# Kernel optimization log

Measured on AMD Instinct MI355X. Metric: run time of the kernel, lower is better.

## Reference

```python
import jax, jax.numpy as jnp
import numpy as np

NEG = -1e9  # effective -inf in log space (finite to keep grads NaN-free)


def _forward_lattice(theta, A):
    """alpha[b,i,j,s]: log-prob of all alignments reaching cell (i,j) in state s.
    States: 0=match (diag move), 1=insert-x (down move), 2=insert-y (right move).
    alpha[i,j,s] = theta[i,j,s] + LSE_k(alpha[i-ds,j-dj,k] + A[k,s]).
    Start: only the match contribution at (0,0) gets log-prob 0."""
    B, N, M, S = theta.shape
    j_is0 = (jnp.arange(M) == 0)  # [M]

    def row_step(prev_row, xs):
        theta_row, i = xs  # theta_row: [B, M, S]
        # diag predecessor alpha[i-1, j-1, :]
        diag = jnp.concatenate(
            [jnp.full((B, 1, S), NEG, theta_row.dtype), prev_row[:, :-1]], axis=1)
        lse_m = jax.nn.logsumexp(diag + A[:, None, :, 0], axis=-1)      # [B, M]
        lse_m = jnp.where((i == 0) & j_is0[None, :], 0.0, lse_m)        # start at (0,0)
        lse_x = jax.nn.logsumexp(prev_row + A[:, None, :, 1], axis=-1)  # [B, M]
        m_vals = theta_row[:, :, 0] + lse_m
        x_vals = theta_row[:, :, 1] + lse_x
        th_y = theta_row[:, :, 2]

        def col_step(left, cxs):
            # left: alpha[i, j-1, :] -> [B, S]
            m_j, x_j, ty_j = cxs  # each [B]
            y_j = ty_j + jax.nn.logsumexp(left + A[:, :, 2], axis=-1)
            cell = jnp.stack([m_j, x_j, y_j], axis=-1)  # [B, S]
            return cell, cell

        left0 = jnp.full((B, S), NEG, theta_row.dtype)
        _, row = jax.lax.scan(col_step, left0, (m_vals.T, x_vals.T, th_y.T))
        row = jnp.transpose(row, (1, 0, 2))  # [B, M, S]
        return row, row

    prev0 = jnp.full((B, M, S), NEG, theta.dtype)
    _, alpha = jax.lax.scan(row_step, prev0, (jnp.swapaxes(theta, 0, 1), jnp.arange(N)))
    return jnp.swapaxes(alpha, 0, 1)  # [B, N, M, S]


def _backward_lattice(theta, A):
    """beta[b,i,j,s]: log-prob of all alignment suffixes from (i,j) in state s.
    beta[i,j,s] = LSE( A[s,0]+theta[i+1,j+1,0]+beta[i+1,j+1,0],
                       A[s,1]+theta[i+1,j,1]  +beta[i+1,j,1],
                       A[s,2]+theta[i,j+1,2]  +beta[i,j+1,2] ),  beta[N-1,M-1,:] = 0.
    Computed as a forward scan on the flipped grid with u = beta + theta."""
    B, N, M, S = theta.shape
    theta_f = theta[:, ::-1, ::-1]
    j_is0 = (jnp.arange(M) == 0)

    def row_step(u_prev, xs):
        th_row, p = xs  # th_row: [B, M, S] (flipped coords)
        t_m = jnp.concatenate(
            [jnp.full((B, 1), NEG, th_row.dtype), u_prev[:, :-1, 0]], axis=1)  # [B, M]
        t_x = u_prev[:, :, 1]  # [B, M]

        def col_step(left_u2, cxs):
            tm_j, tx_j, th_j, j0 = cxs  # [B], [B], [B,S], scalar bool
            v = jnp.stack([tm_j, tx_j, left_u2], axis=-1)     # [B, S] over successor k
            g = jax.nn.logsumexp(A + v[:, None, :], axis=-1)  # [B, S]
            g = jnp.where((p == 0) & j0, 0.0, g)              # terminal cell
            u = g + th_j
            return u[:, 2], (g, u)

        left0 = jnp.full((B,), NEG, th_row.dtype)
        _, (g_row, u_row) = jax.lax.scan(
            col_step, left0, (t_m.T, t_x.T, jnp.swapaxes(th_row, 0, 1), j_is0))
        return jnp.transpose(u_row, (1, 0, 2)), jnp.transpose(g_row, (1, 0, 2))

    u0 = jnp.full((B, M, S), NEG, theta.dtype)
    _, g = jax.lax.scan(row_step, u0, (jnp.swapaxes(theta_f, 0, 1), jnp.arange(N)))
    g = jnp.swapaxes(g, 0, 1)  # [B, N, M, S] flipped coords
    return g[:, ::-1, ::-1]


def setup_inputs() -> dict:
    key = jax.random.key(0)
    k1, k2 = jax.random.split(key)
    B, N, M, S = 256, 128, 128, 3
    theta = jax.random.normal(k1, (B, N, M, S), dtype=jnp.float32)
    A = jax.random.normal(k2, (B, S, S), dtype=jnp.float32)
    return {"theta": theta, "A": A}


def reference(theta, A):
    # Baum-Welch: posterior log-marginals gamma = alpha + beta - logZ
    alpha = _forward_lattice(theta, A)
    beta = _backward_lattice(theta, A)
    logZ = jax.nn.logsumexp(alpha[:, -1, -1, :], axis=-1)  # [B]
    return alpha + beta - logZ[:, None, None, None]
```

## Files before the change

### kernel.cpp

```cpp
#include <hip/hip_runtime.h>

#define HNEG (-1000000000.0f)
#define HNEG2 (-1.44269504e9f)
#define INVLN2 1.44269504088896341f
#define LN2F 0.69314718055994531f

constexpr int Nc = 128;
constexpr int Mc = 128;
constexpr int CELLS = Nc * Mc * 3;

__device__ __forceinline__ float ex2(float x) {
  return __builtin_amdgcn_exp2f(x);
}
__device__ __forceinline__ float lg2(float x) {
  return __builtin_amdgcn_logf(x);
}

__device__ __host__ constexpr int dpoff(int d) {
  return d <= 128 ? (d * (d + 1)) / 2 + ((d + 1) >> 1)
                  : 16448 - ((255 - d) * (256 - d)) / 2 + ((d - 127) >> 1);
}
__device__ __forceinline__ int dlod(int d) { return d > 127 ? d - 127 : 0; }
__device__ __forceinline__ int sidx(int d, int j) {
  const int lo = dlod(d);
  return dpoff(d) + j - lo + (lo & 1);
}
__device__ __forceinline__ int sidx_u(int d) {
  const int lo = dlod(d);
  return dpoff(d) - lo + (lo & 1);
}
constexpr int PCELLS = 16512;
constexpr int PFLOATS = PCELLS * 3;
constexpr int AWSTRIDE = CELLS + 16;

__device__ __forceinline__ float lse3(float a, float b, float c) {
  float mx = fmaxf(fmaxf(a, b), c);
  return mx + __logf(__expf(a - mx) + __expf(b - mx) + __expf(c - mx));
}

__device__ __forceinline__ float shr1f(float src, float fill) {
  return __int_as_float(__builtin_amdgcn_update_dpp(
      __float_as_int(fill), __float_as_int(src), 0x138, 0xF, 0xF, false));
}

__device__ __forceinline__ void st3_even(float* o, float a, float b, float c) {
  *(float2*)o = make_float2(a, b);
  o[2] = c;
}
__device__ __forceinline__ void st3_odd(float* o, float a, float b, float c) {
  o[0] = a;
  *(float2*)(o + 1) = make_float2(b, c);
}

__global__ __launch_bounds__(256) void transpose_kernel(
    const float* __restrict__ theta, float* __restrict__ thd) {
  const int b = blockIdx.x;
  const int tile = blockIdx.y;
  const int i0 = (tile >> 1) * 64, j0 = (tile & 1) * 64;
  const int t = threadIdx.x;
  __shared__ float lds[64 * 192];
  float4* lds4 = (float4*)lds;
  const float4* src4 = (const float4*)(theta + (size_t)b * CELLS);
  float* dst = thd + (size_t)b * PFLOATS;
  const int cbase = (j0 >> 6) * 48;
  for (int f = t; f < 64 * 48; f += 256) {
    const int r = f / 48, c4 = f - r * 48;
    lds4[f] = src4[(size_t)(i0 + r) * 96 + cbase + c4];
  }
  __syncthreads();
  const int g = t >> 6, w = t & 63;
  for (int ld = g; ld < 127; ld += 4) {
    const int d = i0 + j0 + ld;
    const int ljlo = ld > 63 ? ld - 63 : 0;
    const int ljhi = ld < 63 ? ld : 63;
    const int L = (ljhi - ljlo + 1) * 3;
    const int base = sidx(d, j0 + ljlo) * 3;
    for (int e = w; e < L; e += 64) {
      const int lj = ljlo + e / 3, s = e - (e / 3) * 3;
      dst[base + e] = lds[(ld - lj) * 192 + lj * 3 + s] * INVLN2;
    }
  }
}

#define DECL6(p) float p##0, p##1, p##2, p##3, p##4, p##5


#define F2LOAD(P, dd) do {                                                     \
    const int dc_ = (dd) > 254 ? 254 : (dd);                                   \
    const int su_ = __builtin_amdgcn_readfirstlane(sidx_u(dc_));               \
    const float2* p2_ = (const float2*)thd + ((su_ * 3) >> 1) + 3 * l;         \
    const float2 la_ = p2_[0], lb_ = p2_[1], lc_ = p2_[2];                     \
    P##0 = la_.x; P##1 = la_.y; P##2 = lb_.x;                                  \
    P##3 = lb_.y; P##4 = lc_.x; P##5 = lc_.y;                                  \
  } while (0)

#define F2STEP(P, dd) do {                                                     \
    const int iA_ = (dd) - jA, iB_ = (dd) - jB;                                \
    const bool okA_ = (unsigned)iA_ < (unsigned)Nc;                            \
    const bool okB_ = (unsigned)iB_ < (unsigned)Nc;                            \
    const float g0 = mS2 + lg2(wS20 * E00 + wS21 * E10 + wS22 * E20);          \
    const float g1 = mPA + lg2(wPA0 * E01 + wPA1 * E11 + wPA2 * E21);          \
    const float g2 = mS1 + lg2(wS10 * E02 + wS11 * E12 + wS12 * E22);          \
    const float cA0 = okA_ ? P##0 + g0 : HNEG2;                                \
    const float cA1 = okA_ ? P##1 + g1 : HNEG2;                                \
    const float cA2 = okA_ ? P##2 + g2 : HNEG2;                                \
    st3_even(okA_ ? aw + (iA_ * Mc + jA) * 3 : dmpE, cA0, cA1, cA2);           \
    const float h0 = mPP + lg2(wPP0 * E00 + wPP1 * E10 + wPP2 * E20);          \
    const float h1 = mPB + lg2(wPB0 * E01 + wPB1 * E11 + wPB2 * E21);          \
    const float h2 = mPA + lg2(wPA0 * E02 + wPA1 * E12 + wPA2 * E22);          \
    const float cB0 = okB_ ? P##3 + h0 : HNEG2;                                \
    const float cB1 = okB_ ? P##4 + h1 : HNEG2;                                \
    const float cB2 = okB_ ? P##5 + h2 : HNEG2;                                \
    st3_odd(okB_ ? aw + (iB_ * Mc + jB) * 3 : dmpO, cB0, cB1, cB2);            \
    const float mA_ = fmaxf(fmaxf(cA0, cA1), cA2);                             \
    const float a0_ = ex2(cA0 - mA_), a1_ = ex2(cA1 - mA_),                    \
                a2_ = ex2(cA2 - mA_);                                          \
    const float mB_ = fmaxf(fmaxf(cB0, cB1), cB2);                             \
    const float b0_ = ex2(cB0 - mB_), b1_ = ex2(cB1 - mB_),                    \
                b2_ = ex2(cB2 - mB_);                                          \
    mPP = mPA; wPP0 = wPA0; wPP1 = wPA1; wPP2 = wPA2;                          \
    mPA = mA_; wPA0 = a0_; wPA1 = a1_; wPA2 = a2_;                             \
    mPB = mB_; wPB0 = b0_; wPB1 = b1_; wPB2 = b2_;                             \
    mS2 = mS1; wS20 = wS10; wS21 = wS11; wS22 = wS12;                          \
    mS1 = shr1f(mB_, HNEG2);                                                   \
    wS10 = shr1f(b0_, 1.f); wS11 = shr1f(b1_, 1.f); wS12 = shr1f(b2_, 1.f);    \
  } while (0)

#define B2LOADL(Pt, dd) do {                                                   \
    int dor_ = 254 - (dd); if (dor_ < 0) dor_ = 0;                             \
    const int su_ = __builtin_amdgcn_readfirstlane(sidx_u(dor_));              \
    const float2* p2_ =                                                        \
        (const float2*)thd + ((su_ * 3) >> 1) + 3 * (63 - l);                  \
    const float2 la_ = p2_[0], lb_ = p2_[1], lc_ = p2_[2];                     \
    Pt##3 = la_.x; Pt##4 = la_.y; Pt##5 = lb_.x;                               \
    Pt##0 = lb_.y; Pt##1 = lc_.x; Pt##2 = lc_.y;                               \
  } while (0)

#define B2STEPL(Pt, dd) do {                                                   \
    const int iA_ = Nc - 1 - (dd) + jA;                                        \
    const int iB_ = Nc - 1 - (dd) + jB;                                        \
    const bool okA_ = (unsigned)iA_ < (unsigned)Nc;                            \
    const bool okB_ = (unsigned)iB_ < (unsigned)Nc;                            \
    float uA0, uA1, uA2, uB0, uB1, uB2;                                        \
    {                                                                          \
      const float v0 = S2u0, v1 = pAu1, v2 = S1u2;                             \
      const float mv = fmaxf(fmaxf(v0, v1), v2);                               \
      const float w0 = ex2(v0 - mv), w1 = ex2(v1 - mv), w2 = ex2(v2 - mv);     \
      float g0 = mv + lg2(w0 * E00 + w1 * E01 + w2 * E02);                     \
      float g1 = mv + lg2(w0 * E10 + w1 * E11 + w2 * E12);                     \
      float g2 = mv + lg2(w0 * E20 + w1 * E21 + w2 * E22);                     \
      if ((dd) == 0 && l == 0) { g0 = 0.f; g1 = 0.f; g2 = 0.f; }               \
      uA0 = okA_ ? g0 + Pt##0 : HNEG2;                                         \
      uA1 = okA_ ? g1 + Pt##1 : HNEG2;                                         \
      uA2 = okA_ ? g2 + Pt##2 : HNEG2;                                         \
      st3_odd(okA_ ? ob + (iA_ * Mc + jjA) * 3 : dmpO, g0, g1, g2);            \
    }                                                                          \
    {                                                                          \
      const float v0 = ppAu0, v1 = pBu1, v2 = pAu2;                            \
      const float mv = fmaxf(fmaxf(v0, v1), v2);                               \
      const float w0 = ex2(v0 - mv), w1 = ex2(v1 - mv), w2 = ex2(v2 - mv);     \
      const float g0 = mv + lg2(w0 * E00 + w1 * E01 + w2 * E02);               \
      const float g1 = mv + lg2(w0 * E10 + w1 * E11 + w2 * E12);               \
      const float g2 = mv + lg2(w0 * E20 + w1 * E21 + w2 * E22);               \
      uB0 = okB_ ? g0 + Pt##3 : HNEG2;                                         \
      uB1 = okB_ ? g1 + Pt##4 : HNEG2;                                         \
      uB2 = okB_ ? g2 + Pt##5 : HNEG2;                                         \
      st3_even(okB_ ? ob + (iB_ * Mc + jjB) * 3 : dmpE, g0, g1, g2);           \
    }                                                                          \
    ppAu0 = pAu0; pAu0 = uA0; pAu1 = uA1; pAu2 = uA2; pBu1 = uB1;              \
    S2u0 = S1u0;                                                               \
    S1u0 = shr1f(uB0, HNEG2);                                                  \
    S1u2 = shr1f(uB2, HNEG2);                                                  \
  } while (0)

__global__ __launch_bounds__(128, 1) void fb2_kernel(
    const float* __restrict__ thd_, const float* __restrict__ A,
    float* __restrict__ aw_, float* __restrict__ logZ_ws,
    float* __restrict__ ob_) {
  const int b = blockIdx.x;
  const int wave = threadIdx.x >> 6;
  const int l = threadIdx.x & 63;
  const float* thd = thd_ + (size_t)b * PFLOATS;
  const float* Ab = A + b * 9;
  const float E00 = __expf(Ab[0]), E01 = __expf(Ab[1]), E02 = __expf(Ab[2]);
  const float E10 = __expf(Ab[3]), E11 = __expf(Ab[4]), E12 = __expf(Ab[5]);
  const float E20 = __expf(Ab[6]), E21 = __expf(Ab[7]), E22 = __expf(Ab[8]);

  const int jA = 2 * l, jB = 2 * l + 1;
  float* dpad = aw_ + (size_t)b * AWSTRIDE + CELLS;

  if (wave == 0) {
    float* aw = aw_ + (size_t)b * AWSTRIDE;
    float* dmpE = dpad;
    float* dmpO = dpad + 3;

    float mPA = HNEG2, wPA0 = 1.f, wPA1 = 1.f, wPA2 = 1.f;
    float mPB = HNEG2, wPB0 = 1.f, wPB1 = 1.f, wPB2 = 1.f;
    float mPP = HNEG2, wPP0 = 1.f, wPP1 = 1.f, wPP2 = 1.f;
    float mS1 = HNEG2, wS10 = 1.f, wS11 = 1.f, wS12 = 1.f;
    float mS2 = HNEG2, wS20 = 1.f, wS21 = 1.f, wS22 = 1.f;
    if (l == 0) { mS2 = 0.f; wS20 = 1.0f / E00; wS21 = 0.f; wS22 = 0.f; }

    DECL6(xt0); DECL6(xt1); DECL6(xt2); DECL6(xt3);
    DECL6(yt0); DECL6(yt1); DECL6(yt2); DECL6(yt3);

    F2LOAD(xt0, 0); F2LOAD(xt1, 1); F2LOAD(xt2, 2); F2LOAD(xt3, 3);
    F2LOAD(yt0, 4); F2LOAD(yt1, 5); F2LOAD(yt2, 6); F2LOAD(yt3, 7);

    for (int t = 0; t < 31; ++t) {
      const int d0 = 8 * t;
      F2STEP(xt0, d0 + 0); F2STEP(xt1, d0 + 1); F2STEP(xt2, d0 + 2); F2STEP(xt3, d0 + 3);
      F2LOAD(xt0, d0 + 8); F2LOAD(xt1, d0 + 9); F2LOAD(xt2, d0 + 10); F2LOAD(xt3, d0 + 11);
      F2STEP(yt0, d0 + 4); F2STEP(yt1, d0 + 5); F2STEP(yt2, d0 + 6); F2STEP(yt3, d0 + 7);
      F2LOAD(yt0, d0 + 12); F2LOAD(yt1, d0 + 13); F2LOAD(yt2, d0 + 14); F2LOAD(yt3, d0 + 15);
    }
    F2STEP(xt0, 248); F2STEP(xt1, 249); F2STEP(xt2, 250); F2STEP(xt3, 251);
    F2STEP(yt0, 252); F2STEP(yt1, 253); F2STEP(yt2, 254);
    if (l == 63) logZ_ws[b] = mPB + lg2(wPB0 + wPB1 + wPB2);
  } else {
    float* ob = ob_ + (size_t)b * CELLS;
    const int jjA = Mc - 1 - jA, jjB = Mc - 1 - jB;
    float* dmpE = dpad + 8;
    float* dmpO = dpad + 11;

    float pAu0 = HNEG2, pAu1 = HNEG2, pAu2 = HNEG2;
    float ppAu0 = HNEG2, pBu1 = HNEG2;
    float S1u0 = HNEG2, S1u2 = HNEG2, S2u0 = HNEG2;

    DECL6(xt0); DECL6(xt1); DECL6(xt2); DECL6(xt3);
    DECL6(yt0); DECL6(yt1); DECL6(yt2); DECL6(yt3);

    B2LOADL(xt0, 0); B2LOADL(xt1, 1); B2LOADL(xt2, 2); B2LOADL(xt3, 3);
    B2LOADL(yt0, 4); B2LOADL(yt1, 5); B2LOADL(yt2, 6); B2LOADL(yt3, 7);

    for (int t = 0; t < 31; ++t) {
      const int d0 = 8 * t;
      B2STEPL(xt0, d0 + 0); B2STEPL(xt1, d0 + 1);
      B2STEPL(xt2, d0 + 2); B2STEPL(xt3, d0 + 3);
      B2LOADL(xt0, d0 + 8); B2LOADL(xt1, d0 + 9);
      B2LOADL(xt2, d0 + 10); B2LOADL(xt3, d0 + 11);
      B2STEPL(yt0, d0 + 4); B2STEPL(yt1, d0 + 5);
      B2STEPL(yt2, d0 + 6); B2STEPL(yt3, d0 + 7);
      B2LOADL(yt0, d0 + 12); B2LOADL(yt1, d0 + 13);
      B2LOADL(yt2, d0 + 14); B2LOADL(yt3, d0 + 15);
    }
    B2STEPL(xt0, 248); B2STEPL(xt1, 249); B2STEPL(xt2, 250); B2STEPL(xt3, 251);
    B2STEPL(yt0, 252); B2STEPL(yt1, 253); B2STEPL(yt2, 254);
  }
}

__global__ __launch_bounds__(256) void combine_kernel(
    const float4* __restrict__ aw4, const float* __restrict__ logZ_ws,
    float4* __restrict__ out4) {
  const int b = blockIdx.x;
  const float lz = logZ_ws[b];
  const int off = blockIdx.y * 1024 + threadIdx.x;
  const size_t ab = (size_t)b * (AWSTRIDE / 4);
  const size_t obx = (size_t)b * 12288;
#pragma unroll
  for (int k = 0; k < 4; ++k) {
    const size_t i = off + (size_t)k * 256;
    const float4 a = aw4[ab + i];
    const float4 g = out4[obx + i];
    out4[obx + i] =
        make_float4((a.x + g.x - lz) * LN2F, (a.y + g.y - lz) * LN2F,
                    (a.z + g.z - lz) * LN2F, (a.w + g.w - lz) * LN2F);
  }
}

__global__ __launch_bounds__(128) void fwd_fb(const float* __restrict__ theta,
                                              const float* __restrict__ A,
                                              float* __restrict__ out) {
  const int b = blockIdx.x;
  const int j = threadIdx.x;
  const float* th = theta + (size_t)b * CELLS;
  float* ob = out + (size_t)b * CELLS;

  __shared__ float sA[9];
  __shared__ float ring[3][Mc + 1][3];
  if (j < 9) sA[j] = A[b * 9 + j];
  {
    float* rf = &ring[0][0][0];
    for (int t = j; t < 3 * (Mc + 1) * 3; t += Mc) rf[t] = HNEG;
  }
  __syncthreads();
  const float A00 = sA[0], A01 = sA[1], A02 = sA[2];
  const float A10 = sA[3], A11 = sA[4], A12 = sA[5];
  const float A20 = sA[6], A21 = sA[7], A22 = sA[8];

  float p0 = HNEG, p1 = HNEG, p2 = HNEG;
  float tc0 = 0.f, tc1 = 0.f, tc2 = 0.f, tn0 = 0.f, tn1 = 0.f, tn2 = 0.f;
  if (j == 0) { tc0 = th[0]; tc1 = th[1]; tc2 = th[2]; }
  if (j <= 1) {
    const int i1 = 1 - j;
    const float* p = th + (i1 * Mc + j) * 3;
    tn0 = p[0]; tn1 = p[1]; tn2 = p[2];
  }
  int s0 = 0, s1 = 2, s2 = 1;
  for (int d = 0; d < Nc + Mc - 1; ++d) {
    const int i = d - j;
    float tf0 = 0.f, tf1 = 0.f, tf2 = 0.f;
    const int ip = i + 2;
    if (ip >= 0 && ip < Nc) {
      const float* p = th + (ip * Mc + j) * 3;
      tf0 = p[0]; tf1 = p[1]; tf2 = p[2];
    }
    float c0 = HNEG, c1 = HNEG, c2 = HNEG;
    if (i >= 0 && i < Nc) {
      const float* nd1 = ring[s1][j];
      const float* nd2 = ring[s2][j];
      float lm = lse3(nd2[0] + A00, nd2[1] + A10, nd2[2] + A20);
      if (i == 0 && j == 0) lm = 0.0f;
      float lx = lse3(p0 + A01, p1 + A11, p2 + A21);
      float ly = lse3(nd1[0] + A02, nd1[1] + A12, nd1[2] + A22);
      c0 = tc0 + lm; c1 = tc1 + lx; c2 = tc2 + ly;
      float* o = ob + (i * Mc + j) * 3;
      o[0] = c0; o[1] = c1; o[2] = c2;
    }
    float* w = ring[s0][j + 1];
    w[0] = c0; w[1] = c1; w[2] = c2;
    __syncthreads();
    p0 = c0; p1 = c1; p2 = c2;
    tc0 = tn0; tc1 = tn1; tc2 = tn2;
    tn0 = tf0; tn1 = tf1; tn2 = tf2;
    const int t = s2; s2 = s1; s1 = s0; s0 = t;
  }
}

__global__ __launch_bounds__(128) void bwd_fb(const float* __restrict__ theta,
                                              const float* __restrict__ A,
                                              float* __restrict__ ob_) {
  const int b = blockIdx.x;
  const int q = threadIdx.x;
  const float* th = theta + (size_t)b * CELLS;
  float* ob = ob_ + (size_t)b * CELLS;

  __shared__ float sA[9];
  __shared__ float ring[3][Mc + 1][3];
  __shared__ float sZ;
  if (q < 9) sA[q] = A[b * 9 + q];
  {
    float* rf = &ring[0][0][0];
    for (int t = q; t < 3 * (Mc + 1) * 3; t += Mc) rf[t] = HNEG;
  }
  if (q == 0) {
    sZ = lse3(ob[(Nc * Mc - 1) * 3 + 0], ob[(Nc * Mc - 1) * 3 + 1],
              ob[(Nc * Mc - 1) * 3 + 2]);
  }
  __syncthreads();
  const float A00 = sA[0], A01 = sA[1], A02 = sA[2];
  const float A10 = sA[3], A11 = sA[4], A12 = sA[5];
  const float A20 = sA[6], A21 = sA[7], A22 = sA[8];
  const float logZ = sZ;

  const int jj = Mc - 1 - q;
  float pu1 = HNEG;
  float tc0 = 0.f, tc1 = 0.f, tc2 = 0.f, tn0 = 0.f, tn1 = 0.f, tn2 = 0.f;
  float ac0 = 0.f, ac1 = 0.f, ac2 = 0.f, an0 = 0.f, an1 = 0.f, an2 = 0.f;
  if (q == 0) {
    const float* p = th + ((Nc - 1) * Mc + jj) * 3;
    tc0 = p[0]; tc1 = p[1]; tc2 = p[2];
    const float* a = ob + ((Nc - 1) * Mc + jj) * 3;
    ac0 = a[0]; ac1 = a[1]; ac2 = a[2];
  }
  if (q <= 1) {
    const int i1 = Nc - 2 + q;
    const float* p = th + (i1 * Mc + jj) * 3;
    tn0 = p[0]; tn1 = p[1]; tn2 = p[2];
    const float* a = ob + (i1 * Mc + jj) * 3;
    an0 = a[0]; an1 = a[1]; an2 = a[2];
  }
  int s0 = 0, s1 = 2, s2 = 1;
  for (int d = 0; d < Nc + Mc - 1; ++d) {
    const int p = d - q;
    const int i = Nc - 1 - p;
    float tf0 = 0.f, tf1 = 0.f, tf2 = 0.f, af0 = 0.f, af1 = 0.f, af2 = 0.f;
    const int ipf = i - 2;
    if (ipf >= 0 && ipf < Nc) {
      const float* pp = th + (ipf * Mc + jj) * 3;
      tf0 = pp[0]; tf1 = pp[1]; tf2 = pp[2];
      const float* aa = ob + (ipf * Mc + jj) * 3;
      af0 = aa[0]; af1 = aa[1]; af2 = aa[2];
    }
    float u0 = HNEG, u1 = HNEG, u2 = HNEG;
    if (p >= 0 && p < Nc) {
      const float* nd1 = ring[s1][q];
      const float* nd2 = ring[s2][q];
      const float v0 = nd2[0];
      const float v1 = pu1;
      const float v2 = nd1[2];
      float g0 = lse3(A00 + v0, A01 + v1, A02 + v2);
      float g1 = lse3(A10 + v0, A11 + v1, A12 + v2);
      float g2 = lse3(A20 + v0, A21 + v1, A22 + v2);
      if (p == 0 && q == 0) { g0 = 0.0f; g1 = 0.0f; g2 = 0.0f; }
      u0 = g0 + tc0; u1 = g1 + tc1; u2 = g2 + tc2;
      float* o = ob + (i * Mc + jj) * 3;
      o[0] = ac0 + g0 - logZ;
      o[1] = ac1 + g1 - logZ;
      o[2] = ac2 + g2 - logZ;
    }
    float* w = ring[s0][q + 1];
    w[0] = u0; w[1] = u1; w[2] = u2;
    __syncthreads();
    pu1 = u1;
    tc0 = tn0; tc1 = tn1; tc2 = tn2;
    tn0 = tf0; tn1 = tf1; tn2 = tf2;
    ac0 = an0; ac1 = an1; ac2 = an2;
    an0 = af0; an1 = af1; an2 = af2;
    const int t = s2; s2 = s1; s1 = s0; s0 = t;
  }
}

extern "C" void kernel_launch(void* const* d_in, const int* in_sizes, int n_in,
                              void* d_out, int out_size, void* d_ws, size_t ws_size,
                              hipStream_t stream) {
  const float* theta = (const float*)d_in[0];
  const float* A = (const float*)d_in[1];
  float* out = (float*)d_out;
  const int B = in_sizes[1] / 9;

  const size_t need = (size_t)B * (PFLOATS + AWSTRIDE + 1) * 4;
  if (ws_size >= need) {
    float* thd = (float*)d_ws;
    float* aw = thd + (size_t)B * PFLOATS;
    float* logZ_ws = aw + (size_t)B * AWSTRIDE;
    transpose_kernel<<<dim3(B, 4), dim3(256), 0, stream>>>(theta, thd);
    fb2_kernel<<<dim3(B), dim3(128), 0, stream>>>(thd, A, aw, logZ_ws, out);
    combine_kernel<<<dim3(B, 12), dim3(256), 0, stream>>>(
        (const float4*)aw, logZ_ws, (float4*)out);
  } else {
    fwd_fb<<<dim3(B), dim3(128), 0, stream>>>(theta, A, out);
    bwd_fb<<<dim3(B), dim3(128), 0, stream>>>(theta, A, out);
  }
}
```

Measured before the change: 204.0 us.

## Split forward and backward lattice across two waves each with LDS ring handoff

Moves the fused forward/backward kernel from one wave per direction, where each lane handled two columns, to two waves per direction, where each lane handles one column. The second wave runs one 8-diagonal block behind the first and receives boundary column state through a small shared-memory ring buffer. Block-wide barriers after every 8-diagonal block keep the two waves in step. This halves the serial work per lane and doubles the waves per workgroup, at the cost of 33 barriers, LDS traffic, and unaligned scalar stores in place of the paired vector stores.

Result: slower. 211.0 us (+3.4%).

```diff
diff --git a/kernel.cpp b/kernel.cpp
--- a/kernel.cpp
+++ b/kernel.cpp
@@ -41,15 +41,6 @@
 __device__ __forceinline__ float shr1f(float src, float fill) {
   return __int_as_float(__builtin_amdgcn_update_dpp(
       __float_as_int(fill), __float_as_int(src), 0x138, 0xF, 0xF, false));
-}
-
-__device__ __forceinline__ void st3_even(float* o, float a, float b, float c) {
-  *(float2*)o = make_float2(a, b);
-  o[2] = c;
-}
-__device__ __forceinline__ void st3_odd(float* o, float a, float b, float c) {
-  o[0] = a;
-  *(float2*)(o + 1) = make_float2(b, c);
 }
 
 __global__ __launch_bounds__(256) void transpose_kernel(
@@ -82,103 +73,121 @@
   }
 }
 
-#define DECL6(p) float p##0, p##1, p##2, p##3, p##4, p##5
-
-
-#define F2LOAD(P, dd) do {                                                     \
+#define DECL3(p) float p##0, p##1, p##2
+
+
+#define FLOAD(TH, dd) do {                                                     \
     const int dc_ = (dd) > 254 ? 254 : (dd);                                   \
     const int su_ = __builtin_amdgcn_readfirstlane(sidx_u(dc_));               \
-    const float2* p2_ = (const float2*)thd + ((su_ * 3) >> 1) + 3 * l;         \
-    const float2 la_ = p2_[0], lb_ = p2_[1], lc_ = p2_[2];                     \
-    P##0 = la_.x; P##1 = la_.y; P##2 = lb_.x;                                  \
-    P##3 = lb_.y; P##4 = lc_.x; P##5 = lc_.y;                                  \
-  } while (0)
-
-#define F2STEP(P, dd) do {                                                     \
-    const int iA_ = (dd) - jA, iB_ = (dd) - jB;                                \
-    const bool okA_ = (unsigned)iA_ < (unsigned)Nc;                            \
-    const bool okB_ = (unsigned)iB_ < (unsigned)Nc;                            \
-    const float g0 = mS2 + lg2(wS20 * E00 + wS21 * E10 + wS22 * E20);          \
-    const float g1 = mPA + lg2(wPA0 * E01 + wPA1 * E11 + wPA2 * E21);          \
-    const float g2 = mS1 + lg2(wS10 * E02 + wS11 * E12 + wS12 * E22);          \
-    const float cA0 = okA_ ? P##0 + g0 : HNEG2;                                \
-    const float cA1 = okA_ ? P##1 + g1 : HNEG2;                                \
-    const float cA2 = okA_ ? P##2 + g2 : HNEG2;                                \
-    st3_even(okA_ ? aw + (iA_ * Mc + jA) * 3 : dmpE, cA0, cA1, cA2);           \
-    const float h0 = mPP + lg2(wPP0 * E00 + wPP1 * E10 + wPP2 * E20);          \
-    const float h1 = mPB + lg2(wPB0 * E01 + wPB1 * E11 + wPB2 * E21);          \
-    const float h2 = mPA + lg2(wPA0 * E02 + wPA1 * E12 + wPA2 * E22);          \
-    const float cB0 = okB_ ? P##3 + h0 : HNEG2;                                \
-    const float cB1 = okB_ ? P##4 + h1 : HNEG2;                                \
-    const float cB2 = okB_ ? P##5 + h2 : HNEG2;                                \
-    st3_odd(okB_ ? aw + (iB_ * Mc + jB) * 3 : dmpO, cB0, cB1, cB2);            \
-    const float mA_ = fmaxf(fmaxf(cA0, cA1), cA2);                             \
-    const float a0_ = ex2(cA0 - mA_), a1_ = ex2(cA1 - mA_),                    \
-                a2_ = ex2(cA2 - mA_);                                          \
-    const float mB_ = fmaxf(fmaxf(cB0, cB1), cB2);                             \
-    const float b0_ = ex2(cB0 - mB_), b1_ = ex2(cB1 - mB_),                    \
-                b2_ = ex2(cB2 - mB_);                                          \
-    mPP = mPA; wPP0 = wPA0; wPP1 = wPA1; wPP2 = wPA2;                          \
-    mPA = mA_; wPA0 = a0_; wPA1 = a1_; wPA2 = a2_;                             \
-    mPB = mB_; wPB0 = b0_; wPB1 = b1_; wPB2 = b2_;                             \
-    mS2 = mS1; wS20 = wS10; wS21 = wS11; wS22 = wS12;                          \
-    mS1 = shr1f(mB_, HNEG2);                                                   \
-    wS10 = shr1f(b0_, 1.f); wS11 = shr1f(b1_, 1.f); wS12 = shr1f(b2_, 1.f);    \
-  } while (0)
-
-#define B2LOADL(Pt, dd) do {                                                   \
+    const float* p_ = thd + su_ * 3 + 3 * j;                                   \
+    TH##0 = p_[0]; TH##1 = p_[1]; TH##2 = p_[2];                               \
+  } while (0)
+
+#define FSTEP(TH, dd) do {                                                     \
+    float4 hv_;                                                                \
+    if (isB && l == 0) hv_ = *(const float4*)&ringF[(dd) & 31][0];             \
+    const int i_ = (dd) - j;                                                   \
+    const bool ok_ = (unsigned)i_ < (unsigned)Nc;                              \
+    const float g0 = S2m + lg2(S2w0 * E00 + S2w1 * E10 + S2w2 * E20);          \
+    const float g1 = Pm + lg2(Pw0 * E01 + Pw1 * E11 + Pw2 * E21);              \
+    const float g2 = S1m + lg2(S1w0 * E02 + S1w1 * E12 + S1w2 * E22);          \
+    const float c0 = ok_ ? TH##0 + g0 : HNEG2;                                 \
+    const float c1 = ok_ ? TH##1 + g1 : HNEG2;                                 \
+    const float c2 = ok_ ? TH##2 + g2 : HNEG2;                                 \
+    float* o_ = ok_ ? aw + (i_ * Mc + j) * 3 : dmp;                            \
+    o_[0] = c0; o_[1] = c1; o_[2] = c2;                                        \
+    const float m_ = fmaxf(fmaxf(c0, c1), c2);                                 \
+    const float w0_ = ex2(c0 - m_), w1_ = ex2(c1 - m_), w2_ = ex2(c2 - m_);    \
+    if (!isB && l == 63)                                                       \
+      *(float4*)&ringF[(dd) & 31][0] = make_float4(m_, w0_, w1_, w2_);         \
+    S2m = S1m; S2w0 = S1w0; S2w1 = S1w1; S2w2 = S1w2;                          \
+    float nm_ = shr1f(m_, HNEG2);                                              \
+    float n0_ = shr1f(w0_, 1.f), n1_ = shr1f(w1_, 1.f), n2_ = shr1f(w2_, 1.f); \
+    if (isB && l == 0) { nm_ = hv_.x; n0_ = hv_.y; n1_ = hv_.z; n2_ = hv_.w; } \
+    S1m = nm_; S1w0 = n0_; S1w1 = n1_; S1w2 = n2_;                             \
+    Pm = m_; Pw0 = w0_; Pw1 = w1_; Pw2 = w2_;                                  \
+  } while (0)
+
+#define BLOAD(TH, dd) do {                                                     \
     int dor_ = 254 - (dd); if (dor_ < 0) dor_ = 0;                             \
     const int su_ = __builtin_amdgcn_readfirstlane(sidx_u(dor_));              \
-    const float2* p2_ =                                                        \
-        (const float2*)thd + ((su_ * 3) >> 1) + 3 * (63 - l);                  \
-    const float2 la_ = p2_[0], lb_ = p2_[1], lc_ = p2_[2];                     \
-    Pt##3 = la_.x; Pt##4 = la_.y; Pt##5 = lb_.x;                               \
-    Pt##0 = lb_.y; Pt##1 = lc_.x; Pt##2 = lc_.y;                               \
-  } while (0)
-
-#define B2STEPL(Pt, dd) do {                                                   \
-    const int iA_ = Nc - 1 - (dd) + jA;                                        \
-    const int iB_ = Nc - 1 - (dd) + jB;                                        \
-    const bool okA_ = (unsigned)iA_ < (unsigned)Nc;                            \
-    const bool okB_ = (unsigned)iB_ < (unsigned)Nc;                            \
-    float uA0, uA1, uA2, uB0, uB1, uB2;                                        \
-    {                                                                          \
-      const float v0 = S2u0, v1 = pAu1, v2 = S1u2;                             \
-      const float mv = fmaxf(fmaxf(v0, v1), v2);                               \
-      const float w0 = ex2(v0 - mv), w1 = ex2(v1 - mv), w2 = ex2(v2 - mv);     \
-      float g0 = mv + lg2(w0 * E00 + w1 * E01 + w2 * E02);                     \
-      float g1 = mv + lg2(w0 * E10 + w1 * E11 + w2 * E12);                     \
-      float g2 = mv + lg2(w0 * E20 + w1 * E21 + w2 * E22);                     \
-      if ((dd) == 0 && l == 0) { g0 = 0.f; g1 = 0.f; g2 = 0.f; }               \
-      uA0 = okA_ ? g0 + Pt##0 : HNEG2;                                         \
-      uA1 = okA_ ? g1 + Pt##1 : HNEG2;                                         \
-      uA2 = okA_ ? g2 + Pt##2 : HNEG2;                                         \
-      st3_odd(okA_ ? ob + (iA_ * Mc + jjA) * 3 : dmpO, g0, g1, g2);            \
-    }                                                                          \
-    {                                                                          \
-      const float v0 = ppAu0, v1 = pBu1, v2 = pAu2;                            \
-      const float mv = fmaxf(fmaxf(v0, v1), v2);                               \
-      const float w0 = ex2(v0 - mv), w1 = ex2(v1 - mv), w2 = ex2(v2 - mv);     \
-      const float g0 = mv + lg2(w0 * E00 + w1 * E01 + w2 * E02);               \
-      const float g1 = mv + lg2(w0 * E10 + w1 * E11 + w2 * E12);               \
-      const float g2 = mv + lg2(w0 * E20 + w1 * E21 + w2 * E22);               \
-      uB0 = okB_ ? g0 + Pt##3 : HNEG2;                                         \
-      uB1 = okB_ ? g1 + Pt##4 : HNEG2;                                         \
-      uB2 = okB_ ? g2 + Pt##5 : HNEG2;                                         \
-      st3_even(okB_ ? ob + (iB_ * Mc + jjB) * 3 : dmpE, g0, g1, g2);           \
-    }                                                                          \
-    ppAu0 = pAu0; pAu0 = uA0; pAu1 = uA1; pAu2 = uA2; pBu1 = uB1;              \
+    const float* p_ = thd + su_ * 3 + 3 * jj;                                  \
+    TH##0 = p_[0]; TH##1 = p_[1]; TH##2 = p_[2];                               \
+  } while (0)
+
+#define BSTEP(TH, dd) do {                                                     \
+    float2 hv_;                                                                \
+    if (isB && l == 0) hv_ = *(const float2*)&ringB[(dd) & 31][0];             \
+    const int i_ = Nc - 1 - (dd) + q;                                          \
+    const bool ok_ = (unsigned)i_ < (unsigned)Nc;                              \
+    const float v0 = S2u0, v1 = pu1, v2 = S1u2;                                \
+    const float mv = fmaxf(fmaxf(v0, v1), v2);                                 \
+    const float w0_ = ex2(v0 - mv), w1_ = ex2(v1 - mv), w2_ = ex2(v2 - mv);    \
+    float g0 = mv + lg2(w0_ * E00 + w1_ * E01 + w2_ * E02);                    \
+    float g1 = mv + lg2(w0_ * E10 + w1_ * E11 + w2_ * E12);                    \
+    float g2 = mv + lg2(w0_ * E20 + w1_ * E21 + w2_ * E22);                    \
+    if ((dd) == 0 && !isB && l == 0) { g0 = 0.f; g1 = 0.f; g2 = 0.f; }         \
+    const float u0 = ok_ ? g0 + TH##0 : HNEG2;                                 \
+    const float u1 = ok_ ? g1 + TH##1 : HNEG2;                                 \
+    const float u2 = ok_ ? g2 + TH##2 : HNEG2;                                 \
+    float* o_ = ok_ ? ob + (i_ * Mc + jj) * 3 : dmp;                           \
+    o_[0] = g0; o_[1] = g1; o_[2] = g2;                                        \
+    if (!isB && l == 63)                                                       \
+      *(float2*)&ringB[(dd) & 31][0] = make_float2(u0, u2);                    \
+    pu1 = u1;                                                                  \
     S2u0 = S1u0;                                                               \
-    S1u0 = shr1f(uB0, HNEG2);                                                  \
-    S1u2 = shr1f(uB2, HNEG2);                                                  \
-  } while (0)
-
-__global__ __launch_bounds__(128, 1) void fb2_kernel(
+    float n0_ = shr1f(u0, HNEG2), n2_ = shr1f(u2, HNEG2);                      \
+    if (isB && l == 0) { n0_ = hv_.x; n2_ = hv_.y; }                           \
+    S1u0 = n0_; S1u2 = n2_;                                                    \
+  } while (0)
+
+#define FBLK8(D) do {                                                          \
+    FSTEP(x0, (D) + 0); FLOAD(x0, (D) + 8);                                    \
+    FSTEP(x1, (D) + 1); FLOAD(x1, (D) + 9);                                    \
+    FSTEP(x2, (D) + 2); FLOAD(x2, (D) + 10);                                   \
+    FSTEP(x3, (D) + 3); FLOAD(x3, (D) + 11);                                   \
+    FSTEP(x4, (D) + 4); FLOAD(x4, (D) + 12);                                   \
+    FSTEP(x5, (D) + 5); FLOAD(x5, (D) + 13);                                   \
+    FSTEP(x6, (D) + 6); FLOAD(x6, (D) + 14);                                   \
+    FSTEP(x7, (D) + 7); FLOAD(x7, (D) + 15);                                   \
+  } while (0)
+
+#define FBLK7(D) do {                                                          \
+    FSTEP(x0, (D) + 0); FSTEP(x1, (D) + 1); FSTEP(x2, (D) + 2);                \
+    FSTEP(x3, (D) + 3); FSTEP(x4, (D) + 4); FSTEP(x5, (D) + 5);                \
+    FSTEP(x6, (D) + 6);                                                        \
+  } while (0)
+
+#define BBLK8(D) do {                                                          \
+    BSTEP(x0, (D) + 0); BLOAD(x0, (D) + 8);                                    \
+    BSTEP(x1, (D) + 1); BLOAD(x1, (D) + 9);                                    \
+    BSTEP(x2, (D) + 2); BLOAD(x2, (D) + 10);                                   \
+    BSTEP(x3, (D) + 3); BLOAD(x3, (D) + 11);                                   \
+    BSTEP(x4, (D) + 4); BLOAD(x4, (D) + 12);                                   \
+    BSTEP(x5, (D) + 5); BLOAD(x5, (D) + 13);                                   \
+    BSTEP(x6, (D) + 6); BLOAD(x6, (D) + 14);                                   \
+    BSTEP(x7, (D) + 7); BLOAD(x7, (D) + 15);                                   \
+  } while (0)
+
+#define BBLK7(D) do {                                                          \
+    BSTEP(x0, (D) + 0); BSTEP(x1, (D) + 1); BSTEP(x2, (D) + 2);                \
+    BSTEP(x3, (D) + 3); BSTEP(x4, (D) + 4); BSTEP(x5, (D) + 5);                \
+    BSTEP(x6, (D) + 6);                                                        \
+  } while (0)
+
+#define BLOCK_BARRIER() do {                                                   \
+    __builtin_amdgcn_sched_barrier(0);                                         \
+    asm volatile("s_waitcnt lgkmcnt(0)" ::: "memory");                         \
+    __builtin_amdgcn_s_barrier();                                              \
+    __builtin_amdgcn_sched_barrier(0);                                         \
+  } while (0)
+
+__global__ __launch_bounds__(256, 1) void fb4_kernel(
     const float* __restrict__ thd_, const float* __restrict__ A,
     float* __restrict__ aw_, float* __restrict__ logZ_ws,
     float* __restrict__ ob_) {
   const int b = blockIdx.x;
-  const int wave = threadIdx.x >> 6;
+  const int wid = threadIdx.x >> 6;
   const int l = threadIdx.x & 63;
   const float* thd = thd_ + (size_t)b * PFLOATS;
   const float* Ab = A + b * 9;
@@ -186,66 +195,57 @@
   const float E10 = __expf(Ab[3]), E11 = __expf(Ab[4]), E12 = __expf(Ab[5]);
   const float E20 = __expf(Ab[6]), E21 = __expf(Ab[7]), E22 = __expf(Ab[8]);
 
-  const int jA = 2 * l, jB = 2 * l + 1;
-  float* dpad = aw_ + (size_t)b * AWSTRIDE + CELLS;
-
-  if (wave == 0) {
+  __shared__ float ringF[32][4];
+  __shared__ float ringB[32][2];
+
+  float* dmp = aw_ + (size_t)b * AWSTRIDE + CELLS;
+
+  if (wid < 2) {
+    const bool isB = (wid == 1);
+    const int j = (isB ? 64 : 0) + l;
     float* aw = aw_ + (size_t)b * AWSTRIDE;
-    float* dmpE = dpad;
-    float* dmpO = dpad + 3;
-
-    float mPA = HNEG2, wPA0 = 1.f, wPA1 = 1.f, wPA2 = 1.f;
-    float mPB = HNEG2, wPB0 = 1.f, wPB1 = 1.f, wPB2 = 1.f;
-    float mPP = HNEG2, wPP0 = 1.f, wPP1 = 1.f, wPP2 = 1.f;
-    float mS1 = HNEG2, wS10 = 1.f, wS11 = 1.f, wS12 = 1.f;
-    float mS2 = HNEG2, wS20 = 1.f, wS21 = 1.f, wS22 = 1.f;
-    if (l == 0) { mS2 = 0.f; wS20 = 1.0f / E00; wS21 = 0.f; wS22 = 0.f; }
-
-    DECL6(xt0); DECL6(xt1); DECL6(xt2); DECL6(xt3);
-    DECL6(yt0); DECL6(yt1); DECL6(yt2); DECL6(yt3);
-
-    F2LOAD(xt0, 0); F2LOAD(xt1, 1); F2LOAD(xt2, 2); F2LOAD(xt3, 3);
-    F2LOAD(yt0, 4); F2LOAD(yt1, 5); F2LOAD(yt2, 6); F2LOAD(yt3, 7);
-
-    for (int t = 0; t < 31; ++t) {
-      const int d0 = 8 * t;
-      F2STEP(xt0, d0 + 0); F2STEP(xt1, d0 + 1); F2STEP(xt2, d0 + 2); F2STEP(xt3, d0 + 3);
-      F2LOAD(xt0, d0 + 8); F2LOAD(xt1, d0 + 9); F2LOAD(xt2, d0 + 10); F2LOAD(xt3, d0 + 11);
-      F2STEP(yt0, d0 + 4); F2STEP(yt1, d0 + 5); F2STEP(yt2, d0 + 6); F2STEP(yt3, d0 + 7);
-      F2LOAD(yt0, d0 + 12); F2LOAD(yt1, d0 + 13); F2LOAD(yt2, d0 + 14); F2LOAD(yt3, d0 + 15);
-    }
-    F2STEP(xt0, 248); F2STEP(xt1, 249); F2STEP(xt2, 250); F2STEP(xt3, 251);
-    F2STEP(yt0, 252); F2STEP(yt1, 253); F2STEP(yt2, 254);
-    if (l == 63) logZ_ws[b] = mPB + lg2(wPB0 + wPB1 + wPB2);
+
+    float Pm = HNEG2, Pw0 = 1.f, Pw1 = 1.f, Pw2 = 1.f;
+    float S1m = HNEG2, S1w0 = 1.f, S1w1 = 1.f, S1w2 = 1.f;
+    float S2m = HNEG2, S2w0 = 1.f, S2w1 = 1.f, S2w2 = 1.f;
+    if (!isB && l == 0) { S2m = 0.f; S2w0 = 1.0f / E00; S2w1 = 0.f; S2w2 = 0.f; }
+
+    DECL3(x0); DECL3(x1); DECL3(x2); DECL3(x3);
+    DECL3(x4); DECL3(x5); DECL3(x6); DECL3(x7);
+    FLOAD(x0, 0); FLOAD(x1, 1); FLOAD(x2, 2); FLOAD(x3, 3);
+    FLOAD(x4, 4); FLOAD(x5, 5); FLOAD(x6, 6); FLOAD(x7, 7);
+
+    for (int t = 0; t <= 32; ++t) {
+      const bool act = isB ? (t >= 1) : (t < 32);
+      const int D = (isB ? (t - 1) : t) * 8;
+      if (act) {
+        if (D == 248) FBLK7(D); else FBLK8(D);
+      }
+      BLOCK_BARRIER();
+    }
+    if (isB && l == 63) logZ_ws[b] = Pm + lg2(Pw0 + Pw1 + Pw2);
   } else {
+    const bool isB = (wid == 3);
+    const int q = (isB ? 64 : 0) + l;
+    const int jj = Mc - 1 - q;
     float* ob = ob_ + (size_t)b * CELLS;
-    const int jjA = Mc - 1 - jA, jjB = Mc - 1 - jB;
-    float* dmpE = dpad + 8;
-    float* dmpO = dpad + 11;
-
-    float pAu0 = HNEG2, pAu1 = HNEG2, pAu2 = HNEG2;
-    float ppAu0 = HNEG2, pBu1 = HNEG2;
+
+    float pu1 = HNEG2;
     float S1u0 = HNEG2, S1u2 = HNEG2, S2u0 = HNEG2;
 
-    DECL6(xt0); DECL6(xt1); DECL6(xt2); DECL6(xt3);
-    DECL6(yt0); DECL6(yt1); DECL6(yt2); DECL6(yt3);
-
-    B2LOADL(xt0, 0); B2LOADL(xt1, 1); B2LOADL(xt2, 2); B2LOADL(xt3, 3);
-    B2LOADL(yt0, 4); B2LOADL(yt1, 5); B2LOADL(yt2, 6); B2LOADL(yt3, 7);
-
-    for (int t = 0; t < 31; ++t) {
-      const int d0 = 8 * t;
-      B2STEPL(xt0, d0 + 0); B2STEPL(xt1, d0 + 1);
-      B2STEPL(xt2, d0 + 2); B2STEPL(xt3, d0 + 3);
-      B2LOADL(xt0, d0 + 8); B2LOADL(xt1, d0 + 9);
-      B2LOADL(xt2, d0 + 10); B2LOADL(xt3, d0 + 11);
-      B2STEPL(yt0, d0 + 4); B2STEPL(yt1, d0 + 5);
-      B2STEPL(yt2, d0 + 6); B2STEPL(yt3, d0 + 7);
-      B2LOADL(yt0, d0 + 12); B2LOADL(yt1, d0 + 13);
-      B2LOADL(yt2, d0 + 14); B2LOADL(yt3, d0 + 15);
-    }
-    B2STEPL(xt0, 248); B2STEPL(xt1, 249); B2STEPL(xt2, 250); B2STEPL(xt3, 251);
-    B2STEPL(yt0, 252); B2STEPL(yt1, 253); B2STEPL(yt2, 254);
+    DECL3(x0); DECL3(x1); DECL3(x2); DECL3(x3);
+    DECL3(x4); DECL3(x5); DECL3(x6); DECL3(x7);
+    BLOAD(x0, 0); BLOAD(x1, 1); BLOAD(x2, 2); BLOAD(x3, 3);
+    BLOAD(x4, 4); BLOAD(x5, 5); BLOAD(x6, 6); BLOAD(x7, 7);
+
+    for (int t = 0; t <= 32; ++t) {
+      const bool act = isB ? (t >= 1) : (t < 32);
+      const int D = (isB ? (t - 1) : t) * 8;
+      if (act) {
+        if (D == 248) BBLK7(D); else BBLK8(D);
+      }
+      BLOCK_BARRIER();
+    }
   }
 }
 
@@ -425,7 +425,7 @@
     float* aw = thd + (size_t)B * PFLOATS;
     float* logZ_ws = aw + (size_t)B * AWSTRIDE;
     transpose_kernel<<<dim3(B, 4), dim3(256), 0, stream>>>(theta, thd);
-    fb2_kernel<<<dim3(B), dim3(128), 0, stream>>>(thd, A, aw, logZ_ws, out);
+    fb4_kernel<<<dim3(B), dim3(256), 0, stream>>>(thd, A, aw, logZ_ws, out);
     combine_kernel<<<dim3(B, 12), dim3(256), 0, stream>>>(
         (const float4*)aw, logZ_ws, (float4*)out);
   } else {
```

## Fuse transpose and combine into single forward-backward kernel reading theta directly

Applied to the files above, without the earlier changes.

Removes the separate anti-diagonal transpose kernel and the combine kernel, so one kernel per batch element now reads theta straight from its row-major layout using clamped per-lane addresses. The ln-to-log2 scaling is folded into an fma at each step. After both waves finish, logZ is passed through shared memory and the block applies the final alpha+beta-logZ combine itself. This saves two launches and the extra theta copy and intermediate traffic. The cost is strided, uncoalesced theta loads inside the latency-bound scan, and a serial combine tail run by only 128 threads per block.

After: 203.4 us. Within noise of the previous version (-0.3%).

```diff
diff --git a/kernel.cpp b/kernel.cpp
--- a/kernel.cpp
+++ b/kernel.cpp
@@ -8,6 +8,7 @@
 constexpr int Nc = 128;
 constexpr int Mc = 128;
 constexpr int CELLS = Nc * Mc * 3;
+constexpr int AWSTRIDE = CELLS + 16;
 
 __device__ __forceinline__ float ex2(float x) {
   return __builtin_amdgcn_exp2f(x);
@@ -15,23 +16,6 @@
 __device__ __forceinline__ float lg2(float x) {
   return __builtin_amdgcn_logf(x);
 }
-
-__device__ __host__ constexpr int dpoff(int d) {
-  return d <= 128 ? (d * (d + 1)) / 2 + ((d + 1) >> 1)
-                  : 16448 - ((255 - d) * (256 - d)) / 2 + ((d - 127) >> 1);
-}
-__device__ __forceinline__ int dlod(int d) { return d > 127 ? d - 127 : 0; }
-__device__ __forceinline__ int sidx(int d, int j) {
-  const int lo = dlod(d);
-  return dpoff(d) + j - lo + (lo & 1);
-}
-__device__ __forceinline__ int sidx_u(int d) {
-  const int lo = dlod(d);
-  return dpoff(d) - lo + (lo & 1);
-}
-constexpr int PCELLS = 16512;
-constexpr int PFLOATS = PCELLS * 3;
-constexpr int AWSTRIDE = CELLS + 16;
 
 __device__ __forceinline__ float lse3(float a, float b, float c) {
   float mx = fmaxf(fmaxf(a, b), c);
@@ -43,6 +27,10 @@
       __float_as_int(fill), __float_as_int(src), 0x138, 0xF, 0xF, false));
 }
 
+__device__ __forceinline__ int clamp127(int i) {
+  return i < 0 ? 0 : (i > 127 ? 127 : i);
+}
+
 __device__ __forceinline__ void st3_even(float* o, float a, float b, float c) {
   *(float2*)o = make_float2(a, b);
   o[2] = c;
@@ -52,46 +40,16 @@
   *(float2*)(o + 1) = make_float2(b, c);
 }
 
-__global__ __launch_bounds__(256) void transpose_kernel(
-    const float* __restrict__ theta, float* __restrict__ thd) {
-  const int b = blockIdx.x;
-  const int tile = blockIdx.y;
-  const int i0 = (tile >> 1) * 64, j0 = (tile & 1) * 64;
-  const int t = threadIdx.x;
-  __shared__ float lds[64 * 192];
-  float4* lds4 = (float4*)lds;
-  const float4* src4 = (const float4*)(theta + (size_t)b * CELLS);
-  float* dst = thd + (size_t)b * PFLOATS;
-  const int cbase = (j0 >> 6) * 48;
-  for (int f = t; f < 64 * 48; f += 256) {
-    const int r = f / 48, c4 = f - r * 48;
-    lds4[f] = src4[(size_t)(i0 + r) * 96 + cbase + c4];
-  }
-  __syncthreads();
-  const int g = t >> 6, w = t & 63;
-  for (int ld = g; ld < 127; ld += 4) {
-    const int d = i0 + j0 + ld;
-    const int ljlo = ld > 63 ? ld - 63 : 0;
-    const int ljhi = ld < 63 ? ld : 63;
-    const int L = (ljhi - ljlo + 1) * 3;
-    const int base = sidx(d, j0 + ljlo) * 3;
-    for (int e = w; e < L; e += 64) {
-      const int lj = ljlo + e / 3, s = e - (e / 3) * 3;
-      dst[base + e] = lds[(ld - lj) * 192 + lj * 3 + s] * INVLN2;
-    }
-  }
-}
-
 #define DECL6(p) float p##0, p##1, p##2, p##3, p##4, p##5
 
 
 #define F2LOAD(P, dd) do {                                                     \
     const int dc_ = (dd) > 254 ? 254 : (dd);                                   \
-    const int su_ = __builtin_amdgcn_readfirstlane(sidx_u(dc_));               \
-    const float2* p2_ = (const float2*)thd + ((su_ * 3) >> 1) + 3 * l;         \
-    const float2 la_ = p2_[0], lb_ = p2_[1], lc_ = p2_[2];                     \
-    P##0 = la_.x; P##1 = la_.y; P##2 = lb_.x;                                  \
-    P##3 = lb_.y; P##4 = lc_.x; P##5 = lc_.y;                                  \
+    const int ca_ = clamp127(dc_ - jA), cb_ = clamp127(dc_ - jB);              \
+    const float* pa_ = th + (ca_ * Mc + jA) * 3;                               \
+    const float* pb_ = th + (cb_ * Mc + jB) * 3;                               \
+    P##0 = pa_[0]; P##1 = pa_[1]; P##2 = pa_[2];                               \
+    P##3 = pb_[0]; P##4 = pb_[1]; P##5 = pb_[2];                               \
   } while (0)
 
 #define F2STEP(P, dd) do {                                                     \
@@ -101,16 +59,16 @@
     const float g0 = mS2 + lg2(wS20 * E00 + wS21 * E10 + wS22 * E20);          \
     const float g1 = mPA + lg2(wPA0 * E01 + wPA1 * E11 + wPA2 * E21);          \
     const float g2 = mS1 + lg2(wS10 * E02 + wS11 * E12 + wS12 * E22);          \
-    const float cA0 = okA_ ? P##0 + g0 : HNEG2;                                \
-    const float cA1 = okA_ ? P##1 + g1 : HNEG2;                                \
-    const float cA2 = okA_ ? P##2 + g2 : HNEG2;                                \
+    const float cA0 = okA_ ? fmaf(P##0, INVLN2, g0) : HNEG2;                   \
+    const float cA1 = okA_ ? fmaf(P##1, INVLN2, g1) : HNEG2;                   \
+    const float cA2 = okA_ ? fmaf(P##2, INVLN2, g2) : HNEG2;                   \
     st3_even(okA_ ? aw + (iA_ * Mc + jA) * 3 : dmpE, cA0, cA1, cA2);           \
     const float h0 = mPP + lg2(wPP0 * E00 + wPP1 * E10 + wPP2 * E20);          \
     const float h1 = mPB + lg2(wPB0 * E01 + wPB1 * E11 + wPB2 * E21);          \
     const float h2 = mPA + lg2(wPA0 * E02 + wPA1 * E12 + wPA2 * E22);          \
-    const float cB0 = okB_ ? P##3 + h0 : HNEG2;                                \
-    const float cB1 = okB_ ? P##4 + h1 : HNEG2;                                \
-    const float cB2 = okB_ ? P##5 + h2 : HNEG2;                                \
+    const float cB0 = okB_ ? fmaf(P##3, INVLN2, h0) : HNEG2;                   \
+    const float cB1 = okB_ ? fmaf(P##4, INVLN2, h1) : HNEG2;                   \
+    const float cB2 = okB_ ? fmaf(P##5, INVLN2, h2) : HNEG2;                   \
     st3_odd(okB_ ? aw + (iB_ * Mc + jB) * 3 : dmpO, cB0, cB1, cB2);            \
     const float mA_ = fmaxf(fmaxf(cA0, cA1), cA2);                             \
     const float a0_ = ex2(cA0 - mA_), a1_ = ex2(cA1 - mA_),                    \
@@ -128,12 +86,11 @@
 
 #define B2LOADL(Pt, dd) do {                                                   \
     int dor_ = 254 - (dd); if (dor_ < 0) dor_ = 0;                             \
-    const int su_ = __builtin_amdgcn_readfirstlane(sidx_u(dor_));              \
-    const float2* p2_ =                                                        \
-        (const float2*)thd + ((su_ * 3) >> 1) + 3 * (63 - l);                  \
-    const float2 la_ = p2_[0], lb_ = p2_[1], lc_ = p2_[2];                     \
-    Pt##3 = la_.x; Pt##4 = la_.y; Pt##5 = lb_.x;                               \
-    Pt##0 = lb_.y; Pt##1 = lc_.x; Pt##2 = lc_.y;                               \
+    const int ca_ = clamp127(dor_ - jjA), cb_ = clamp127(dor_ - jjB);          \
+    const float* pa_ = th + (ca_ * Mc + jjA) * 3;                              \
+    const float* pb_ = th + (cb_ * Mc + jjB) * 3;                              \
+    Pt##0 = pa_[0]; Pt##1 = pa_[1]; Pt##2 = pa_[2];                            \
+    Pt##3 = pb_[0]; Pt##4 = pb_[1]; Pt##5 = pb_[2];                            \
   } while (0)
 
 #define B2STEPL(Pt, dd) do {                                                   \
@@ -150,9 +107,9 @@
       float g1 = mv + lg2(w0 * E10 + w1 * E11 + w2 * E12);                     \
       float g2 = mv + lg2(w0 * E20 + w1 * E21 + w2 * E22);                     \
       if ((dd) == 0 && l == 0) { g0 = 0.f; g1 = 0.f; g2 = 0.f; }               \
-      uA0 = okA_ ? g0 + Pt##0 : HNEG2;                                         \
-      uA1 = okA_ ? g1 + Pt##1 : HNEG2;                                         \
-      uA2 = okA_ ? g2 + Pt##2 : HNEG2;                                         \
+      uA0 = okA_ ? fmaf(Pt##0, INVLN2, g0) : HNEG2;                            \
+      uA1 = okA_ ? fmaf(Pt##1, INVLN2, g1) : HNEG2;                            \
+      uA2 = okA_ ? fmaf(Pt##2, INVLN2, g2) : HNEG2;                            \
       st3_odd(okA_ ? ob + (iA_ * Mc + jjA) * 3 : dmpO, g0, g1, g2);            \
     }                                                                          \
     {                                                                          \
@@ -162,9 +119,9 @@
       const float g0 = mv + lg2(w0 * E00 + w1 * E01 + w2 * E02);               \
       const float g1 = mv + lg2(w0 * E10 + w1 * E11 + w2 * E12);               \
       const float g2 = mv + lg2(w0 * E20 + w1 * E21 + w2 * E22);               \
-      uB0 = okB_ ? g0 + Pt##3 : HNEG2;                                         \
-      uB1 = okB_ ? g1 + Pt##4 : HNEG2;                                         \
-      uB2 = okB_ ? g2 + Pt##5 : HNEG2;                                         \
+      uB0 = okB_ ? fmaf(Pt##3, INVLN2, g0) : HNEG2;                            \
+      uB1 = okB_ ? fmaf(Pt##4, INVLN2, g1) : HNEG2;                            \
+      uB2 = okB_ ? fmaf(Pt##5, INVLN2, g2) : HNEG2;                            \
       st3_even(okB_ ? ob + (iB_ * Mc + jjB) * 3 : dmpE, g0, g1, g2);           \
     }                                                                          \
     ppAu0 = pAu0; pAu0 = uA0; pAu1 = uA1; pAu2 = uA2; pBu1 = uB1;              \
@@ -173,24 +130,26 @@
     S1u2 = shr1f(uB2, HNEG2);                                                  \
   } while (0)
 
-__global__ __launch_bounds__(128, 1) void fb2_kernel(
-    const float* __restrict__ thd_, const float* __restrict__ A,
-    float* __restrict__ aw_, float* __restrict__ logZ_ws,
-    float* __restrict__ ob_) {
+__global__ __launch_bounds__(128, 1) void fbf_kernel(
+    const float* __restrict__ theta, const float* __restrict__ A,
+    float* __restrict__ aw_, float* __restrict__ ob_) {
   const int b = blockIdx.x;
   const int wave = threadIdx.x >> 6;
   const int l = threadIdx.x & 63;
-  const float* thd = thd_ + (size_t)b * PFLOATS;
+  const float* th = theta + (size_t)b * CELLS;
   const float* Ab = A + b * 9;
   const float E00 = __expf(Ab[0]), E01 = __expf(Ab[1]), E02 = __expf(Ab[2]);
   const float E10 = __expf(Ab[3]), E11 = __expf(Ab[4]), E12 = __expf(Ab[5]);
   const float E20 = __expf(Ab[6]), E21 = __expf(Ab[7]), E22 = __expf(Ab[8]);
 
+  __shared__ float sLZ;
+
   const int jA = 2 * l, jB = 2 * l + 1;
-  float* dpad = aw_ + (size_t)b * AWSTRIDE + CELLS;
+  float* aw = aw_ + (size_t)b * AWSTRIDE;
+  float* ob = ob_ + (size_t)b * CELLS;
+  float* dpad = aw + CELLS;
 
   if (wave == 0) {
-    float* aw = aw_ + (size_t)b * AWSTRIDE;
     float* dmpE = dpad;
     float* dmpO = dpad + 3;
 
@@ -216,9 +175,8 @@
     }
     F2STEP(xt0, 248); F2STEP(xt1, 249); F2STEP(xt2, 250); F2STEP(xt3, 251);
     F2STEP(yt0, 252); F2STEP(yt1, 253); F2STEP(yt2, 254);
-    if (l == 63) logZ_ws[b] = mPB + lg2(wPB0 + wPB1 + wPB2);
+    if (l == 63) sLZ = mPB + lg2(wPB0 + wPB1 + wPB2);
   } else {
-    float* ob = ob_ + (size_t)b * CELLS;
     const int jjA = Mc - 1 - jA, jjB = Mc - 1 - jB;
     float* dmpE = dpad + 8;
     float* dmpO = dpad + 11;
@@ -247,24 +205,17 @@
     B2STEPL(xt0, 248); B2STEPL(xt1, 249); B2STEPL(xt2, 250); B2STEPL(xt3, 251);
     B2STEPL(yt0, 252); B2STEPL(yt1, 253); B2STEPL(yt2, 254);
   }
-}
-
-__global__ __launch_bounds__(256) void combine_kernel(
-    const float4* __restrict__ aw4, const float* __restrict__ logZ_ws,
-    float4* __restrict__ out4) {
-  const int b = blockIdx.x;
-  const float lz = logZ_ws[b];
-  const int off = blockIdx.y * 1024 + threadIdx.x;
-  const size_t ab = (size_t)b * (AWSTRIDE / 4);
-  const size_t obx = (size_t)b * 12288;
-#pragma unroll
-  for (int k = 0; k < 4; ++k) {
-    const size_t i = off + (size_t)k * 256;
-    const float4 a = aw4[ab + i];
-    const float4 g = out4[obx + i];
-    out4[obx + i] =
-        make_float4((a.x + g.x - lz) * LN2F, (a.y + g.y - lz) * LN2F,
-                    (a.z + g.z - lz) * LN2F, (a.w + g.w - lz) * LN2F);
+
+  __syncthreads();
+  const float lz = sLZ;
+  const float4* a4 = (const float4*)aw;
+  float4* o4 = (float4*)ob;
+#pragma unroll 4
+  for (int k = threadIdx.x; k < CELLS / 4; k += 128) {
+    const float4 a = a4[k];
+    const float4 g = o4[k];
+    o4[k] = make_float4((a.x + g.x - lz) * LN2F, (a.y + g.y - lz) * LN2F,
+                        (a.z + g.z - lz) * LN2F, (a.w + g.w - lz) * LN2F);
   }
 }
 
@@ -419,15 +370,10 @@
   float* out = (float*)d_out;
   const int B = in_sizes[1] / 9;
 
-  const size_t need = (size_t)B * (PFLOATS + AWSTRIDE + 1) * 4;
+  const size_t need = (size_t)B * AWSTRIDE * 4;
   if (ws_size >= need) {
-    float* thd = (float*)d_ws;
-    float* aw = thd + (size_t)B * PFLOATS;
-    float* logZ_ws = aw + (size_t)B * AWSTRIDE;
-    transpose_kernel<<<dim3(B, 4), dim3(256), 0, stream>>>(theta, thd);
-    fb2_kernel<<<dim3(B), dim3(128), 0, stream>>>(thd, A, aw, logZ_ws, out);
-    combine_kernel<<<dim3(B, 12), dim3(256), 0, stream>>>(
-        (const float4*)aw, logZ_ws, (float4*)out);
+    float* aw = (float*)d_ws;
+    fbf_kernel<<<dim3(B), dim3(128), 0, stream>>>(theta, A, aw, out);
   } else {
     fwd_fb<<<dim3(B), dim3(128), 0, stream>>>(theta, A, out);
     bwd_fb<<<dim3(B), dim3(128), 0, stream>>>(theta, A, out);
```
